# Kernel tuning notes

Measured on AMD Instinct MI355X. Metric: run time of the kernel, lower is better.

## Reference

```python
import jax, jax.numpy as jnp
import numpy as np

E = 8           # num_experts
K = 2           # num_experts_per_tok
D = 1024        # hidden_size
F = 2048        # intermediate_dim
B, S = 1, 2048  # batch, seq_len


def setup_inputs() -> dict:
    key = jax.random.key(0)
    k0, k1, k2, k3, k4, k5 = jax.random.split(key, 6)
    hidden_states = jax.random.normal(k0, (B, S, D), dtype=jnp.float32)
    topk_weights = jax.random.uniform(k1, (B * S, K), dtype=jnp.float32)
    topk_ids = jax.random.randint(k2, (B * S, K), 0, E, dtype=jnp.int32)
    scale = 0.02
    wi_0 = jax.random.normal(k3, (E, D, F), dtype=jnp.float32) * scale
    wi_1 = jax.random.normal(k4, (E, D, F), dtype=jnp.float32) * scale
    wo = jax.random.normal(k5, (E, F, D), dtype=jnp.float32) * scale
    return {"hidden_states": hidden_states, "topk_weights": topk_weights,
            "topk_ids": topk_ids, "wi_0": wi_0, "wi_1": wi_1, "wo": wo}


def _gmm(x, w, group_sizes):
    """Grouped matmul: rows of x are sorted by expert; group_sizes[e] rows use w[e].
    Small fixed loop over experts (E=8); rows not owned by expert e are masked out."""
    n_e = w.shape[0]
    expert_of_row = jnp.repeat(jnp.arange(n_e), group_sizes,
                               total_repeat_length=x.shape[0])  # [M]
    out = jnp.zeros((x.shape[0], w.shape[2]), dtype=x.dtype)
    for e in range(n_e):
        out = out + jnp.where((expert_of_row == e)[:, None], x @ w[e], 0.0)
    return out


def _moe_forward(hidden_states, topk_weights, topk_ids, wi_0, wi_1, wo):
    b, s, d = hidden_states.shape
    k = topk_ids.shape[1]
    n_e = wi_0.shape[0]
    x2d = hidden_states.reshape(b * s, d)

    # ---- permute: sort expanded tokens by selected expert (stable) ----
    flat_experts = jnp.ravel(topk_ids)                       # [T*K]
    sort_idx = jnp.argsort(flat_experts, stable=True)        # [T*K]
    sorted_rows = sort_idx // k                              # source token per row
    x_sorted = jnp.take(x2d, sorted_rows, axis=0)            # [T*K, D]
    group_sizes = jnp.bincount(flat_experts, length=n_e)     # [E]

    # ---- grouped GEMMs with SwiGLU (gate * up, then down) ----
    g0 = _gmm(x_sorted, wi_0, group_sizes)                   # [T*K, F]
    g1 = _gmm(x_sorted, wi_1, group_sizes)                   # [T*K, F]
    h = jax.nn.silu(g0) * g1                                 # fused SiLU-gate
    y = _gmm(h, wo, group_sizes)                             # [T*K, D]

    # ---- unpermute and combine with routing weights (fp32 accum) ----
    unsort_idx = jnp.argsort(sort_idx, stable=True)
    y = jnp.take(y, unsort_idx, axis=0).reshape(b * s, k, d)
    out = jnp.einsum('bke,bk->be', y.astype(jnp.float32),
                     topk_weights.astype(jnp.float32))
    return out.reshape(b, s, d)


def reference(hidden_states, topk_weights, topk_ids, wi_0, wi_1, wo):
    return _moe_forward(hidden_states, topk_weights, topk_ids, wi_0, wi_1, wo)
```

## Files before the change

### kernel.cpp

```cpp
#include <hip/hip_runtime.h>
#include <hip/hip_bf16.h>


#define D_DIM 1024
#define F_DIM 2048
#define ROWS 4096
#define MAXTILE 40
#define LDK 72

using f32x4 = __attribute__((ext_vector_type(4))) float;
using s16x8 = __attribute__((ext_vector_type(8))) short;

__device__ __forceinline__ unsigned pack_trunc(float lo, float hi) {
  return (__float_as_uint(lo) >> 16) | (__float_as_uint(hi) & 0xffff0000u);
}
__device__ __forceinline__ unsigned short bf_rn(float f) {
  unsigned u = __float_as_uint(f);
  u += 0x7fffu + ((u >> 16) & 1u);
  return (unsigned short)(u >> 16);
}
__device__ __forceinline__ unsigned pack_rn(float lo, float hi) {
  return (unsigned)bf_rn(lo) | ((unsigned)bf_rn(hi) << 16);
}

typedef const __attribute__((address_space(1))) void* gp_t;
typedef __attribute__((address_space(3))) void* lp_t;
__device__ __forceinline__ void load16(const void* g, void* l) {
  __builtin_amdgcn_global_load_lds((gp_t)g, (lp_t)l, 16, 0, 0);
}

__global__ __launch_bounds__(512) void route_kernel(const int* __restrict__ ids,
                                                    int* __restrict__ sorted_flat,
                                                    int* __restrict__ unsort,
                                                    int* __restrict__ tile_meta) {
  __shared__ int sid[ROWS];
  __shared__ int cnt[8];
  __shared__ int off[9];
  const int tid = threadIdx.x;
#pragma unroll
  for (int j = 0; j < 2; j++) {
    int idx = tid + j * 512;
    *(int4*)&sid[idx * 4] = *(const int4*)&ids[idx * 4];
  }
  __syncthreads();
  const int w = tid >> 6, lane = tid & 63;
  int c = 0;
  for (int base = 0; base < ROWS; base += 64)
    c += __popcll(__ballot(sid[base + lane] == w));
  if (lane == 0) cnt[w] = c;
  __syncthreads();
  if (tid == 0) {
    int o = 0;
    for (int e = 0; e < 8; e++) { off[e] = o; o += cnt[e]; }
    off[8] = o;
    int nT = 0;
    for (int e = 0; e < 8; e++) {
      for (int r0 = off[e]; r0 < off[e + 1]; r0 += 128) {
        tile_meta[1 + 3 * nT] = r0;
        tile_meta[2 + 3 * nT] = off[e + 1];
        tile_meta[3 + 3 * nT] = e;
        nT++;
      }
    }
    tile_meta[0] = nT;
  }
  __syncthreads();
  int pos = off[w];
  const unsigned long long below = (1ull << lane) - 1ull;
  for (int base = 0; base < ROWS; base += 64) {
    unsigned long long m = __ballot(sid[base + lane] == w);
    if (sid[base + lane] == w) {
      int p = pos + __popcll(m & below);
      sorted_flat[p] = base + lane;
      unsort[base + lane] = p;
    }
    pos += __popcll(m);
  }
}

__global__ void zero_kernel(float4* __restrict__ p, int n4) {
  int i = blockIdx.x * blockDim.x + threadIdx.x;
  if (i < n4) p[i] = float4{0.f, 0.f, 0.f, 0.f};
}

__global__ __launch_bounds__(512, 4) void convT_lds(
    const float* __restrict__ wi0, const float* __restrict__ wi1,
    const float* __restrict__ wo, unsigned short* __restrict__ w0T,
    unsigned short* __restrict__ w1T, unsigned short* __restrict__ woT) {
  __shared__ unsigned t[128 * 128];
  const int z = blockIdx.y;
  const int which = z >> 3, e = z & 7;
  const float* S;
  unsigned short* Dp;
  int Kd, Nd, nbits;
  if (which == 0)      { S = wi0; Dp = w0T; Kd = D_DIM; Nd = F_DIM; nbits = 4; }
  else if (which == 1) { S = wi1; Dp = w1T; Kd = D_DIM; Nd = F_DIM; nbits = 4; }
  else                 { S = wo;  Dp = woT; Kd = F_DIM; Nd = D_DIM; nbits = 3; }
  S  += (size_t)e * Kd * Nd;
  Dp += (size_t)e * Kd * Nd;
  const int n0 = (blockIdx.x & ((1 << nbits) - 1)) * 128;
  const int k0 = (blockIdx.x >> nbits) * 256;
  const int tid = threadIdx.x;
  const int nc  = tid & 31;
  const int kpb = tid >> 5;

  float4 v[8][2];
#pragma unroll
  for (int r = 0; r < 8; r++) {
    const int kp = kpb + r * 16;
    const float* p = S + (size_t)(k0 + 2 * kp) * Nd + n0 + nc * 4;
    v[r][0] = *(const float4*)p;
    v[r][1] = *(const float4*)(p + Nd);
  }
  __builtin_amdgcn_sched_barrier(0);

#pragma unroll
  for (int r = 0; r < 8; r++) {
    const int kp = kpb + r * 16;
    const int q = kp >> 2, ql = kp & 3;
    const int col = ((q ^ (nc & 7)) << 2) | ql;
    t[(4 * nc + 0) * 128 + col] = pack_rn(v[r][0].x, v[r][1].x);
    t[(4 * nc + 1) * 128 + col] = pack_rn(v[r][0].y, v[r][1].y);
    t[(4 * nc + 2) * 128 + col] = pack_rn(v[r][0].z, v[r][1].z);
    t[(4 * nc + 3) * 128 + col] = pack_rn(v[r][0].w, v[r][1].w);
  }
  __syncthreads();

  const int c = tid & 31;
#pragma unroll
  for (int s = 0; s < 8; s++) {
    const int n = (tid >> 5) + s * 16;
    const int col = (c ^ ((n >> 2) & 7)) << 2;
    const unsigned* qp = &t[n * 128 + col];
    uint4 o = make_uint4(qp[0], qp[1], qp[2], qp[3]);
    *(uint4*)(Dp + (size_t)(n0 + n) * Kd + k0 + c * 8) = o;
  }
}

__global__ __launch_bounds__(256) void gather_kernel(const float* __restrict__ x,
                                                     const int* __restrict__ sorted_flat,
                                                     unsigned short* __restrict__ xs) {
  const int r = blockIdx.x;
  const int tok = sorted_flat[r] >> 1;
  const float4 v = *(const float4*)(x + (size_t)tok * D_DIM + threadIdx.x * 4);
  *(uint2*)(xs + (size_t)r * D_DIM + threadIdx.x * 4) =
      make_uint2(pack_rn(v.x, v.y), pack_rn(v.z, v.w));
}

__device__ __forceinline__ int sw(int row, int chunk) {
  return row * 64 + ((chunk ^ (row & 7)) << 3);
}

__global__ __launch_bounds__(256, 3) void gemm1_kernel(
    const unsigned short* __restrict__ xs, const unsigned short* __restrict__ w0T,
    const unsigned short* __restrict__ w1T, const int* __restrict__ tile_meta,
    unsigned short* __restrict__ h) {
  __shared__ unsigned short As[128 * 64];
  __shared__ unsigned short B0s[64 * 64];
  __shared__ unsigned short B1s[64 * 64];
  const int tile = blockIdx.x;
  if (tile >= tile_meta[0]) return;
  const int row0 = tile_meta[1 + 3 * tile];
  const int rowEnd = tile_meta[2 + 3 * tile];
  const int e = tile_meta[3 + 3 * tile];
  const int n0 = blockIdx.y * 64;
  const unsigned short* W0 = w0T + ((size_t)e * F_DIM + n0) * D_DIM;
  const unsigned short* W1 = w1T + ((size_t)e * F_DIM + n0) * D_DIM;

  const int tid = threadIdx.x;
  const int lane = tid & 63, wv = tid >> 6;
  const int wm = (wv & 1) * 64, wn = (wv >> 1) * 32;
  const int lm = lane & 15, lq = lane >> 4;
  const int srow = lane >> 3;
  const int skk = ((lane & 7) ^ srow) << 3;

  f32x4 acc0[4][2], acc1[4][2];
#pragma unroll
  for (int i = 0; i < 4; i++)
#pragma unroll
    for (int j = 0; j < 2; j++) { acc0[i][j] = 0.f; acc1[i][j] = 0.f; }

  for (int k0 = 0; k0 < D_DIM; k0 += 64) {
    __syncthreads();
#pragma unroll
    for (int r = 0; r < 4; r++) {
      const int c = r * 4 + wv;
      const int m = c * 8 + srow;
      int mc = row0 + m; if (mc > ROWS - 1) mc = ROWS - 1;
      load16(xs + (size_t)mc * D_DIM + k0 + skk, (char*)As + c * 1024);
    }
#pragma unroll
    for (int r = 0; r < 2; r++) {
      const int c = r * 4 + wv;
      const int m = c * 8 + srow;
      load16(W0 + (size_t)m * D_DIM + k0 + skk, (char*)B0s + c * 1024);
      load16(W1 + (size_t)m * D_DIM + k0 + skk, (char*)B1s + c * 1024);
    }
    __syncthreads();
#pragma unroll
    for (int ks = 0; ks < 64; ks += 32) {
      const int cb = (ks >> 3) + lq;
      s16x8 af[4], b0[2], b1[2];
#pragma unroll
      for (int t = 0; t < 4; t++)
        af[t] = *(const s16x8*)&As[sw(wm + t * 16 + lm, cb)];
#pragma unroll
      for (int t = 0; t < 2; t++) {
        b0[t] = *(const s16x8*)&B0s[sw(wn + t * 16 + lm, cb)];
        b1[t] = *(const s16x8*)&B1s[sw(wn + t * 16 + lm, cb)];
      }
#pragma unroll
      for (int im = 0; im < 4; im++)
#pragma unroll
        for (int in = 0; in < 2; in++) {
          acc0[im][in] = __builtin_amdgcn_mfma_f32_16x16x32_bf16(
              af[im], b0[in], acc0[im][in], 0, 0, 0);
          acc1[im][in] = __builtin_amdgcn_mfma_f32_16x16x32_bf16(
              af[im], b1[in], acc1[im][in], 0, 0, 0);
        }
    }
  }
#pragma unroll
  for (int im = 0; im < 4; im++) {
    int gmB = row0 + wm + im * 16 + lq * 4;
#pragma unroll
    for (int in = 0; in < 2; in++) {
      int gn = n0 + wn + in * 16 + lm;
#pragma unroll
      for (int r = 0; r < 4; r++) {
        int gm = gmB + r;
        if (gm < rowEnd) {
          float g = acc0[im][in][r];
          float s = g / (1.f + __expf(-g));
          h[(size_t)gm * F_DIM + gn] = bf_rn(s * acc1[im][in][r]);
        }
      }
    }
  }
}

__global__ __launch_bounds__(256, 4) void gemm2_kernel(
    const unsigned short* __restrict__ h, const unsigned short* __restrict__ woT,
    const int* __restrict__ tile_meta, float* __restrict__ y) {
  __shared__ unsigned short As[128 * 64];
  __shared__ unsigned short Bs[64 * 64];
  const int tile = blockIdx.x;
  if (tile >= tile_meta[0]) return;
  const int row0 = tile_meta[1 + 3 * tile];
  const int rowEnd = tile_meta[2 + 3 * tile];
  const int e = tile_meta[3 + 3 * tile];
  const int n0 = blockIdx.y * 64;
  const unsigned short* W = woT + ((size_t)e * D_DIM + n0) * F_DIM;

  const int tid = threadIdx.x;
  const int lane = tid & 63, wv = tid >> 6;
  const int wm = (wv & 1) * 64, wn = (wv >> 1) * 32;
  const int lm = lane & 15, lq = lane >> 4;
  const int srow = lane >> 3;
  const int skk = ((lane & 7) ^ srow) << 3;

  f32x4 acc[4][2];
#pragma unroll
  for (int i = 0; i < 4; i++)
#pragma unroll
    for (int j = 0; j < 2; j++) acc[i][j] = 0.f;

  for (int k0 = 0; k0 < F_DIM; k0 += 64) {
    __syncthreads();
#pragma unroll
    for (int r = 0; r < 4; r++) {
      const int c = r * 4 + wv;
      const int m = c * 8 + srow;
      int mc = row0 + m; if (mc > ROWS - 1) mc = ROWS - 1;
      load16(h + (size_t)mc * F_DIM + k0 + skk, (char*)As + c * 1024);
    }
#pragma unroll
    for (int r = 0; r < 2; r++) {
      const int c = r * 4 + wv;
      const int m = c * 8 + srow;
      load16(W + (size_t)m * F_DIM + k0 + skk, (char*)Bs + c * 1024);
    }
    __syncthreads();
#pragma unroll
    for (int ks = 0; ks < 64; ks += 32) {
      const int cb = (ks >> 3) + lq;
      s16x8 af[4], bf[2];
#pragma unroll
      for (int t = 0; t < 4; t++)
        af[t] = *(const s16x8*)&As[sw(wm + t * 16 + lm, cb)];
#pragma unroll
      for (int t = 0; t < 2; t++)
        bf[t] = *(const s16x8*)&Bs[sw(wn + t * 16 + lm, cb)];
#pragma unroll
      for (int im = 0; im < 4; im++)
#pragma unroll
        for (int in = 0; in < 2; in++)
          acc[im][in] = __builtin_amdgcn_mfma_f32_16x16x32_bf16(
              af[im], bf[in], acc[im][in], 0, 0, 0);
    }
  }
#pragma unroll
  for (int im = 0; im < 4; im++) {
    int gmB = row0 + wm + im * 16 + lq * 4;
#pragma unroll
    for (int in = 0; in < 2; in++) {
      int gn = n0 + wn + in * 16 + lm;
#pragma unroll
      for (int r = 0; r < 4; r++) {
        int gm = gmB + r;
        if (gm < rowEnd) y[(size_t)gm * D_DIM + gn] = acc[im][in][r];
      }
    }
  }
}

__global__ __launch_bounds__(256) void combine_kernel(const float* __restrict__ y,
                                                      const float* __restrict__ tw,
                                                      const int* __restrict__ unsort,
                                                      float* __restrict__ out) {
  const int tkn = blockIdx.x;
  const int r0 = unsort[2 * tkn], r1 = unsort[2 * tkn + 1];
  const float w0 = tw[2 * tkn], w1 = tw[2 * tkn + 1];
  const int c = threadIdx.x * 4;
  float4 a = *(const float4*)(y + (size_t)r0 * D_DIM + c);
  float4 b = *(const float4*)(y + (size_t)r1 * D_DIM + c);
  float4 o = {w0 * a.x + w1 * b.x, w0 * a.y + w1 * b.y,
              w0 * a.z + w1 * b.z, w0 * a.w + w1 * b.w};
  *(float4*)(out + (size_t)tkn * D_DIM + c) = o;
}

__device__ __forceinline__ void stage_bt(const float* __restrict__ Wt, int ldw,
                                         unsigned short* Bs, int tid) {
#pragma unroll
  for (int it = 0; it < 4; it++) {
    const int kp = (tid & 7) + it * 8;
    const int nq = tid >> 3;
    const float* p = Wt + (size_t)(2 * kp) * ldw + nq * 4;
    const float4 va = *(const float4*)p;
    const float4 vb = *(const float4*)(p + ldw);
    unsigned short* b = Bs + (nq * 4) * LDK + 2 * kp;
    *(unsigned*)(b)           = pack_trunc(va.x, vb.x);
    *(unsigned*)(b + LDK)     = pack_trunc(va.y, vb.y);
    *(unsigned*)(b + 2 * LDK) = pack_trunc(va.z, vb.z);
    *(unsigned*)(b + 3 * LDK) = pack_trunc(va.w, vb.w);
  }
}

__global__ __launch_bounds__(256, 2) void gemm1_fb(
    const float* __restrict__ x, const float* __restrict__ wi0,
    const float* __restrict__ wi1, const int* __restrict__ sorted_flat,
    const int* __restrict__ tile_meta, unsigned short* __restrict__ h) {
  __shared__ unsigned short As[128 * LDK];
  __shared__ unsigned short B0s[128 * LDK];
  __shared__ unsigned short B1s[128 * LDK];
  __shared__ int tok[128];
  const int tile = blockIdx.x;
  if (tile >= tile_meta[0]) return;
  const int row0 = tile_meta[1 + 3 * tile];
  const int rowEnd = tile_meta[2 + 3 * tile];
  const int e = tile_meta[3 + 3 * tile];
  const int n0 = blockIdx.y * 128;
  const float* W0 = wi0 + (size_t)e * D_DIM * F_DIM;
  const float* W1 = wi1 + (size_t)e * D_DIM * F_DIM;
  const int tid = threadIdx.x;
  if (tid < 128) {
    int r = row0 + tid; if (r > ROWS - 1) r = ROWS - 1;
    tok[tid] = sorted_flat[r] >> 1;
  }
  f32x4 acc0[4][4], acc1[4][4];
#pragma unroll
  for (int i = 0; i < 4; i++)
#pragma unroll
    for (int j = 0; j < 4; j++) { acc0[i][j] = 0.f; acc1[i][j] = 0.f; }
  const int lane = tid & 63, wv = tid >> 6;
  const int wm = (wv & 1) * 64, wn = (wv >> 1) * 64;
  const int lm = lane & 15, lq = lane >> 4;
  for (int k0 = 0; k0 < D_DIM; k0 += 64) {
    __syncthreads();
#pragma unroll
    for (int i = 0; i < 8; i++) {
      int idx = tid + i * 256;
      int m = idx >> 4, kq = idx & 15;
      float4 v = *(const float4*)(x + (size_t)tok[m] * D_DIM + k0 + kq * 4);
      *(uint2*)&As[m * LDK + kq * 4] =
          make_uint2(pack_trunc(v.x, v.y), pack_trunc(v.z, v.w));
    }
    stage_bt(W0 + (size_t)k0 * F_DIM + n0, F_DIM, B0s, tid);
    stage_bt(W1 + (size_t)k0 * F_DIM + n0, F_DIM, B1s, tid);
    __syncthreads();
#pragma unroll
    for (int ks = 0; ks < 64; ks += 32) {
      s16x8 af[4], b0[4], b1[4];
#pragma unroll
      for (int t = 0; t < 4; t++) {
        af[t] = *(const s16x8*)&As[(wm + t * 16 + lm) * LDK + ks + lq * 8];
        b0[t] = *(const s16x8*)&B0s[(wn + t * 16 + lm) * LDK + ks + lq * 8];
        b1[t] = *(const s16x8*)&B1s[(wn + t * 16 + lm) * LDK + ks + lq * 8];
      }
#pragma unroll
      for (int im = 0; im < 4; im++)
#pragma unroll
        for (int in = 0; in < 4; in++) {
          acc0[im][in] = __builtin_amdgcn_mfma_f32_16x16x32_bf16(
              af[im], b0[in], acc0[im][in], 0, 0, 0);
          acc1[im][in] = __builtin_amdgcn_mfma_f32_16x16x32_bf16(
              af[im], b1[in], acc1[im][in], 0, 0, 0);
        }
    }
  }
#pragma unroll
  for (int im = 0; im < 4; im++) {
    int gmB = row0 + wm + im * 16 + lq * 4;
#pragma unroll
    for (int in = 0; in < 4; in++) {
      int gn = n0 + wn + in * 16 + lm;
#pragma unroll
      for (int r = 0; r < 4; r++) {
        int gm = gmB + r;
        if (gm < rowEnd) {
          float g = acc0[im][in][r];
          float s = g / (1.f + __expf(-g));
          h[(size_t)gm * F_DIM + gn] = bf_rn(s * acc1[im][in][r]);
        }
      }
    }
  }
}

__global__ __launch_bounds__(256, 3) void gemm2_fb(
    const unsigned short* __restrict__ h, const float* __restrict__ wo,
    const float* __restrict__ tw, const int* __restrict__ sorted_flat,
    const int* __restrict__ tile_meta, float* __restrict__ out) {
  __shared__ unsigned short As[128 * LDK];
  __shared__ unsigned short Bs[128 * LDK];
  __shared__ int sTok[128];
  __shared__ float sWgt[128];
  const int tile = blockIdx.x;
  if (tile >= tile_meta[0]) return;
  const int row0 = tile_meta[1 + 3 * tile];
  const int rowEnd = tile_meta[2 + 3 * tile];
  const int e = tile_meta[3 + 3 * tile];
  const int n0 = blockIdx.y * 128;
  const float* W = wo + (size_t)e * F_DIM * D_DIM;
  const int tid = threadIdx.x;
  if (tid < 128) {
    int r = row0 + tid; if (r > ROWS - 1) r = ROWS - 1;
    int fl = sorted_flat[r];
    sTok[tid] = fl >> 1;
    sWgt[tid] = tw[fl];
  }
  f32x4 acc[4][4];
#pragma unroll
  for (int i = 0; i < 4; i++)
#pragma unroll
    for (int j = 0; j < 4; j++) acc[i][j] = 0.f;
  const int lane = tid & 63, wv = tid >> 6;
  const int wm = (wv & 1) * 64, wn = (wv >> 1) * 64;
  const int lm = lane & 15, lq = lane >> 4;
  for (int k0 = 0; k0 < F_DIM; k0 += 64) {
    __syncthreads();
#pragma unroll
    for (int i = 0; i < 8; i++) {
      int idx = tid + i * 256;
      int m = idx >> 4, kq = idx & 15;
      int gm = row0 + m; if (gm > ROWS - 1) gm = ROWS - 1;
      *(uint2*)&As[m * LDK + kq * 4] =
          *(const uint2*)(h + (size_t)gm * F_DIM + k0 + kq * 4);
    }
    stage_bt(W + (size_t)k0 * D_DIM + n0, D_DIM, Bs, tid);
    __syncthreads();
#pragma unroll
    for (int ks = 0; ks < 64; ks += 32) {
      s16x8 af[4], bf[4];
#pragma unroll
      for (int t = 0; t < 4; t++) {
        af[t] = *(const s16x8*)&As[(wm + t * 16 + lm) * LDK + ks + lq * 8];
        bf[t] = *(const s16x8*)&Bs[(wn + t * 16 + lm) * LDK + ks + lq * 8];
      }
#pragma unroll
      for (int im = 0; im < 4; im++)
#pragma unroll
        for (int in = 0; in < 4; in++)
          acc[im][in] = __builtin_amdgcn_mfma_f32_16x16x32_bf16(
              af[im], bf[in], acc[im][in], 0, 0, 0);
    }
  }
#pragma unroll
  for (int im = 0; im < 4; im++) {
    int lrB = wm + im * 16 + lq * 4;
#pragma unroll
    for (int in = 0; in < 4; in++) {
      int gn = n0 + wn + in * 16 + lm;
#pragma unroll
      for (int r = 0; r < 4; r++) {
        int lr = lrB + r;
        int gm = row0 + lr;
        if (gm < rowEnd)
          atomicAdd(out + (size_t)sTok[lr] * D_DIM + gn, sWgt[lr] * acc[im][in][r]);
      }
    }
  }
}

extern "C" void kernel_launch(void* const* d_in, const int* in_sizes, int n_in,
                              void* d_out, int out_size, void* d_ws, size_t ws_size,
                              hipStream_t stream) {
  const float* x   = (const float*)d_in[0];
  const float* tw  = (const float*)d_in[1];
  const int*   ids = (const int*)d_in[2];
  const float* wi0 = (const float*)d_in[3];
  const float* wi1 = (const float*)d_in[4];
  const float* wo  = (const float*)d_in[5];
  float* out = (float*)d_out;

  int* tile_meta = (int*)d_ws;
  int* sorted_flat = tile_meta + 256;
  int* unsort = sorted_flat + ROWS;

  const size_t MB = 1024 * 1024;
  const size_t XS_OFF = 64 * 1024;
  const size_t H_OFF  = XS_OFF + 8 * MB;
  const size_t W0_OFF = H_OFF + 16 * MB;
  const size_t W1_OFF = W0_OFF + 32 * MB;
  const size_t WO_OFF = W1_OFF + 32 * MB;
  const size_t NEED   = WO_OFF + 32 * MB;

  route_kernel<<<1, 512, 0, stream>>>(ids, sorted_flat, unsort, tile_meta);
  if (ws_size >= NEED) {
    unsigned short* xs  = (unsigned short*)((char*)d_ws + XS_OFF);
    unsigned short* h   = (unsigned short*)((char*)d_ws + H_OFF);
    unsigned short* w0T = (unsigned short*)((char*)d_ws + W0_OFF);
    unsigned short* w1T = (unsigned short*)((char*)d_ws + W1_OFF);
    unsigned short* woT = (unsigned short*)((char*)d_ws + WO_OFF);
    float* y = (float*)((char*)d_ws + W0_OFF);

    convT_lds<<<dim3(64, 24), 512, 0, stream>>>(wi0, wi1, wo, w0T, w1T, woT);
    gather_kernel<<<ROWS, 256, 0, stream>>>(x, sorted_flat, xs);
    gemm1_kernel<<<dim3(MAXTILE, F_DIM / 64), 256, 0, stream>>>(xs, w0T, w1T,
                                                                tile_meta, h);
    gemm2_kernel<<<dim3(MAXTILE, D_DIM / 64), 256, 0, stream>>>(h, woT,
                                                                tile_meta, y);
    combine_kernel<<<ROWS / 2, 256, 0, stream>>>(y, tw, unsort, out);
  } else {
    unsigned short* h = (unsigned short*)((char*)d_ws + XS_OFF);
    zero_kernel<<<(out_size / 4 + 255) / 256, 256, 0, stream>>>((float4*)out,
                                                                out_size / 4);
    gemm1_fb<<<dim3(MAXTILE, F_DIM / 128), 256, 0, stream>>>(x, wi0, wi1,
                                                             sorted_flat,
                                                             tile_meta, h);
    gemm2_fb<<<dim3(MAXTILE, D_DIM / 128), 256, 0, stream>>>(h, wo, tw,
                                                             sorted_flat,
                                                             tile_meta, out);
  }
}
```

Measured before the change: 319.9 us.

## Fold routing and output zeroing into convT, fuse combine into gemm2 via atomics

The routing kernel and the zeroing of the output now run as extra block rows inside the weight-transpose kernel, which removes two separate launches. The combine kernel is gone: gemm2 now scales each row by its routing weight and atomically adds it into the output at the row's source token, so the fp32 intermediate y is never written or read back. In exchange, every output element takes two float atomic adds, which also makes the summation order nondeterministic. The weight transpose still runs on every call.

```diff
diff --git a/kernel.cpp b/kernel.cpp
--- a/kernel.cpp
+++ b/kernel.cpp
@@ -29,13 +29,11 @@
   __builtin_amdgcn_global_load_lds((gp_t)g, (lp_t)l, 16, 0, 0);
 }
 
-__global__ __launch_bounds__(512) void route_kernel(const int* __restrict__ ids,
-                                                    int* __restrict__ sorted_flat,
-                                                    int* __restrict__ unsort,
-                                                    int* __restrict__ tile_meta) {
-  __shared__ int sid[ROWS];
-  __shared__ int cnt[8];
-  __shared__ int off[9];
+__device__ __forceinline__ void route_body(const int* __restrict__ ids,
+                                           int* __restrict__ sorted_flat,
+                                           int* __restrict__ unsort,
+                                           int* __restrict__ tile_meta,
+                                           int* sid, int* cnt, int* off) {
   const int tid = threadIdx.x;
 #pragma unroll
   for (int j = 0; j < 2; j++) {
@@ -78,6 +76,16 @@
   }
 }
 
+__global__ __launch_bounds__(512) void route_kernel(const int* __restrict__ ids,
+                                                    int* __restrict__ sorted_flat,
+                                                    int* __restrict__ unsort,
+                                                    int* __restrict__ tile_meta) {
+  __shared__ int sid[ROWS];
+  __shared__ int cnt[8];
+  __shared__ int off[9];
+  route_body(ids, sorted_flat, unsort, tile_meta, sid, cnt, off);
+}
+
 __global__ void zero_kernel(float4* __restrict__ p, int n4) {
   int i = blockIdx.x * blockDim.x + threadIdx.x;
   if (i < n4) p[i] = float4{0.f, 0.f, 0.f, 0.f};
@@ -86,9 +94,24 @@
 __global__ __launch_bounds__(512, 4) void convT_lds(
     const float* __restrict__ wi0, const float* __restrict__ wi1,
     const float* __restrict__ wo, unsigned short* __restrict__ w0T,
-    unsigned short* __restrict__ w1T, unsigned short* __restrict__ woT) {
+    unsigned short* __restrict__ w1T, unsigned short* __restrict__ woT,
+    const int* __restrict__ ids, int* __restrict__ sorted_flat,
+    int* __restrict__ unsort, int* __restrict__ tile_meta,
+    float4* __restrict__ out4) {
   __shared__ unsigned t[128 * 128];
   const int z = blockIdx.y;
+  if (z == 24) {
+    if (blockIdx.x != 0) return;
+    route_body(ids, sorted_flat, unsort, tile_meta,
+               (int*)t, (int*)&t[4096], (int*)&t[4104]);
+    return;
+  }
+  if (z == 25) {
+    const int n4 = (ROWS / 2) * D_DIM / 4;
+    for (int i = blockIdx.x * 512 + threadIdx.x; i < n4; i += 64 * 512)
+      out4[i] = float4{0.f, 0.f, 0.f, 0.f};
+    return;
+  }
   const int which = z >> 3, e = z & 7;
   const float* S;
   unsigned short* Dp;
@@ -241,9 +264,12 @@
 
 __global__ __launch_bounds__(256, 4) void gemm2_kernel(
     const unsigned short* __restrict__ h, const unsigned short* __restrict__ woT,
-    const int* __restrict__ tile_meta, float* __restrict__ y) {
+    const float* __restrict__ tw, const int* __restrict__ sorted_flat,
+    const int* __restrict__ tile_meta, float* __restrict__ out) {
   __shared__ unsigned short As[128 * 64];
   __shared__ unsigned short Bs[64 * 64];
+  __shared__ int sTok[128];
+  __shared__ float sWgt[128];
   const int tile = blockIdx.x;
   if (tile >= tile_meta[0]) return;
   const int row0 = tile_meta[1 + 3 * tile];
@@ -253,6 +279,12 @@
   const unsigned short* W = woT + ((size_t)e * D_DIM + n0) * F_DIM;
 
   const int tid = threadIdx.x;
+  if (tid < 128) {
+    int r = row0 + tid; if (r > ROWS - 1) r = ROWS - 1;
+    int fl = sorted_flat[r];
+    sTok[tid] = fl >> 1;
+    sWgt[tid] = tw[fl];
+  }
   const int lane = tid & 63, wv = tid >> 6;
   const int wm = (wv & 1) * 64, wn = (wv >> 1) * 32;
   const int lm = lane & 15, lq = lane >> 4;
@@ -301,32 +333,20 @@
   }
 #pragma unroll
   for (int im = 0; im < 4; im++) {
-    int gmB = row0 + wm + im * 16 + lq * 4;
+    int lrB = wm + im * 16 + lq * 4;
 #pragma unroll
     for (int in = 0; in < 2; in++) {
       int gn = n0 + wn + in * 16 + lm;
 #pragma unroll
       for (int r = 0; r < 4; r++) {
-        int gm = gmB + r;
-        if (gm < rowEnd) y[(size_t)gm * D_DIM + gn] = acc[im][in][r];
-      }
-    }
-  }
-}
-
-__global__ __launch_bounds__(256) void combine_kernel(const float* __restrict__ y,
-                                                      const float* __restrict__ tw,
-                                                      const int* __restrict__ unsort,
-                                                      float* __restrict__ out) {
-  const int tkn = blockIdx.x;
-  const int r0 = unsort[2 * tkn], r1 = unsort[2 * tkn + 1];
-  const float w0 = tw[2 * tkn], w1 = tw[2 * tkn + 1];
-  const int c = threadIdx.x * 4;
-  float4 a = *(const float4*)(y + (size_t)r0 * D_DIM + c);
-  float4 b = *(const float4*)(y + (size_t)r1 * D_DIM + c);
-  float4 o = {w0 * a.x + w1 * b.x, w0 * a.y + w1 * b.y,
-              w0 * a.z + w1 * b.z, w0 * a.w + w1 * b.w};
-  *(float4*)(out + (size_t)tkn * D_DIM + c) = o;
+        int lr = lrB + r;
+        int gm = row0 + lr;
+        if (gm < rowEnd)
+          atomicAdd(out + (size_t)sTok[lr] * D_DIM + gn,
+                    sWgt[lr] * acc[im][in][r]);
+      }
+    }
+  }
 }
 
 __device__ __forceinline__ void stage_bt(const float* __restrict__ Wt, int ldw,
@@ -525,26 +545,27 @@
   const size_t WO_OFF = W1_OFF + 32 * MB;
   const size_t NEED   = WO_OFF + 32 * MB;
 
-  route_kernel<<<1, 512, 0, stream>>>(ids, sorted_flat, unsort, tile_meta);
   if (ws_size >= NEED) {
     unsigned short* xs  = (unsigned short*)((char*)d_ws + XS_OFF);
     unsigned short* h   = (unsigned short*)((char*)d_ws + H_OFF);
     unsigned short* w0T = (unsigned short*)((char*)d_ws + W0_OFF);
     unsigned short* w1T = (unsigned short*)((char*)d_ws + W1_OFF);
     unsigned short* woT = (unsigned short*)((char*)d_ws + WO_OFF);
-    float* y = (float*)((char*)d_ws + W0_OFF);
-
-    convT_lds<<<dim3(64, 24), 512, 0, stream>>>(wi0, wi1, wo, w0T, w1T, woT);
+
+    convT_lds<<<dim3(64, 26), 512, 0, stream>>>(wi0, wi1, wo, w0T, w1T, woT,
+                                                ids, sorted_flat, unsort,
+                                                tile_meta, (float4*)out);
     gather_kernel<<<ROWS, 256, 0, stream>>>(x, sorted_flat, xs);
     gemm1_kernel<<<dim3(MAXTILE, F_DIM / 64), 256, 0, stream>>>(xs, w0T, w1T,
                                                                 tile_meta, h);
-    gemm2_kernel<<<dim3(MAXTILE, D_DIM / 64), 256, 0, stream>>>(h, woT,
-                                                                tile_meta, y);
-    combine_kernel<<<ROWS / 2, 256, 0, stream>>>(y, tw, unsort, out);
+    gemm2_kernel<<<dim3(MAXTILE, D_DIM / 64), 256, 0, stream>>>(h, woT, tw,
+                                                                sorted_flat,
+                                                                tile_meta, out);
   } else {
     unsigned short* h = (unsigned short*)((char*)d_ws + XS_OFF);
-    zero_kernel<<<(out_size / 4 + 255) / 256, 256, 0, stream>>>((float4*)out,
-                                                                out_size / 4);
+    route_kernel<<<1, 512, 0, stream>>>(ids, sorted_flat, unsort, tile_meta);
+    zero_kernel<<<(ROWS / 2 * D_DIM / 4 + 255) / 256, 256, 0, stream>>>(
+        (float4*)out, ROWS / 2 * D_DIM / 4);
     gemm1_fb<<<dim3(MAXTILE, F_DIM / 128), 256, 0, stream>>>(x, wi0, wi1,
                                                              sorted_flat,
                                                              tile_meta, h);
```

New measurement: 315.4 us. About the same (-1.4%).
